# Kernel optimization log

Hardware: AMD Instinct MI355X
Metric: run time of the kernel (lower is better)

Reference implementation:

```python
import jax, jax.numpy as jnp
import numpy as np

N_SRC0, N_DST0 = 100000, 20000   # block0: 100k src -> 20k dst
N_DST1 = 4096                    # block1: 20k src -> 4096 dst (seed nodes)


def setup_inputs() -> dict:
    key = jax.random.key(0)
    ks = jax.random.split(key, 8)
    E0, E1 = 640000, 131072
    return {
        "features": jax.random.normal(ks[0], (N_SRC0, 256), jnp.float32),
        "W1": jax.random.normal(ks[1], (256, 256), jnp.float32) * (1.0 / np.sqrt(256)),
        "b1": jnp.zeros((256,), jnp.float32),
        "W2": jax.random.normal(ks[2], (256, 128), jnp.float32) * (1.0 / np.sqrt(256)),
        "b2": jnp.zeros((128,), jnp.float32),
        "src0": jax.random.randint(ks[3], (E0,), 0, N_SRC0, jnp.int32),
        "dst0": jax.random.randint(ks[4], (E0,), 0, N_DST0, jnp.int32),
        "src1": jax.random.randint(ks[5], (E1,), 0, N_DST0, jnp.int32),
        "dst1": jax.random.randint(ks[6], (E1,), 0, N_DST1, jnp.int32),
    }


def _graph_conv(src, dst, n_dst, feat, W, b):
    # DGL GraphConv, norm='both': D_out^{-1/2} gather-sum D_in^{-1/2}, then WX+b.
    n_src = feat.shape[0]
    ones = jnp.ones(src.shape[0], feat.dtype)
    out_deg = jax.ops.segment_sum(ones, src, num_segments=n_src)
    norm_src = jnp.clip(out_deg, 1.0, None) ** -0.5          # [n_src]
    h = feat * norm_src[:, None]
    agg = jax.ops.segment_sum(h[src], dst, num_segments=n_dst)  # sparse SpMM
    in_deg = jax.ops.segment_sum(ones, dst, num_segments=n_dst)
    norm_dst = jnp.clip(in_deg, 1.0, None) ** -0.5           # [n_dst]
    return (agg * norm_dst[:, None]) @ W + b


def reference(features, W1, b1, W2, b2, src0, dst0, src1, dst1):
    x = jax.nn.relu(_graph_conv(src0, dst0, N_DST0, features, W1, b1))
    x = _graph_conv(src1, dst1, N_DST1, x, W2, b2)
    return x
```

## Files before the change

kernel.cpp:

```cpp
#include <hip/hip_runtime.h>
#include <hip/hip_bf16.h>

#define K_DIM 256
#define RSTRIDE 128
#define EPB 8192

#define G0_DB 625
#define G0_SB 256
#define G0_SW 392
#define G1_DB 128
#define G1_SB 64
#define G1_SW 313

#define NB_FIN (G0_DB + G1_DB + G0_SB + G1_SB)

typedef short bf16x8 __attribute__((ext_vector_type(8)));
typedef float f32x4 __attribute__((ext_vector_type(4)));

static __device__ __forceinline__ unsigned short f2bf(float x) {
    __hip_bfloat16 b = __float2bfloat16(x);
    return *reinterpret_cast<unsigned short*>(&b);
}
static __device__ __forceinline__ float bflo(unsigned int p) {
    return __uint_as_float(p << 16);
}
static __device__ __forceinline__ float bfhi(unsigned int p) {
    return __uint_as_float(p & 0xffff0000u);
}

static __device__ __forceinline__ void block_exscan(
        const int* __restrict__ hist, int* __restrict__ offs, int* __restrict__ tmp, int M) {
    const int tid = threadIdx.x;
    const int S = (M + 255) >> 8;
    const int base = tid * S;
    int sum = 0;
    for (int k = 0; k < S; ++k) {
        int idx = base + k;
        if (idx < M) sum += hist[idx];
    }
    tmp[tid] = sum;
    __syncthreads();
    for (int d = 1; d < 256; d <<= 1) {
        int v = tmp[tid];
        int u = (tid >= d) ? tmp[tid - d] : 0;
        __syncthreads();
        tmp[tid] = v + u;
        __syncthreads();
    }
    int run = (tid == 0) ? 0 : tmp[tid - 1];
    for (int k = 0; k < S; ++k) {
        int idx = base + k;
        if (idx < M) { offs[idx] = run; run += hist[idx]; }
    }
    __syncthreads();
}

struct SplitSh {
    int hist[640];
    int offs[640];
    int tmp[256];
    unsigned sorted[EPB];
};

template <int NDB, int NSB, int SW>
static __device__ __forceinline__ void split_sort(
        const int* __restrict__ src, const int* __restrict__ dst, int E, int chunk,
        int* __restrict__ cntD, int* __restrict__ offD,
        int* __restrict__ cntS, int* __restrict__ offS,
        unsigned* __restrict__ sortD, unsigned* __restrict__ sortS, SplitSh& sh) {
    const int tid = threadIdx.x;
    const int e0 = chunk * EPB;
    const int n = min(EPB, E - e0);
    for (int i = tid; i < NDB; i += 256) sh.hist[i] = 0;
    __syncthreads();
    for (int j = tid; j < n; j += 256) atomicAdd(&sh.hist[dst[e0 + j] >> 5], 1);
    __syncthreads();
    block_exscan(sh.hist, sh.offs, sh.tmp, NDB);
    for (int i = tid; i < NDB; i += 256) {
        cntD[chunk * NDB + i] = sh.hist[i];
        offD[chunk * NDB + i] = sh.offs[i];
    }
    __syncthreads();
    for (int j = tid; j < n; j += 256) {
        int d = dst[e0 + j];
        int s = src[e0 + j];
        int pos = atomicAdd(&sh.offs[d >> 5], 1);
        sh.sorted[pos] = ((unsigned)s << 5) | (unsigned)(d & 31);
    }
    __syncthreads();
    {
        unsigned* __restrict__ gout = sortD + (size_t)chunk * EPB;
        for (int j = tid; j < n; j += 256) gout[j] = sh.sorted[j];
    }
    __syncthreads();
    for (int i = tid; i < NSB; i += 256) sh.hist[i] = 0;
    __syncthreads();
    for (int j = tid; j < n; j += 256)
        atomicAdd(&sh.hist[(int)((unsigned)src[e0 + j] / SW)], 1);
    __syncthreads();
    block_exscan(sh.hist, sh.offs, sh.tmp, NSB);
    for (int i = tid; i < NSB; i += 256) {
        cntS[chunk * NSB + i] = sh.hist[i];
        offS[chunk * NSB + i] = sh.offs[i];
    }
    __syncthreads();
    for (int j = tid; j < n; j += 256) {
        unsigned s = (unsigned)src[e0 + j];
        int pos = atomicAdd(&sh.offs[s / SW], 1);
        sh.sorted[pos] = s;
    }
    __syncthreads();
    {
        unsigned* __restrict__ gout = sortS + (size_t)chunk * EPB;
        for (int j = tid; j < n; j += 256) gout[j] = sh.sorted[j];
    }
}

__global__ __launch_bounds__(256) void splitA_kernel(
        const int* __restrict__ src0, const int* __restrict__ dst0, int E0,
        const int* __restrict__ src1, const int* __restrict__ dst1, int E1,
        int* __restrict__ cntD0, int* __restrict__ offD0,
        int* __restrict__ cntS0, int* __restrict__ offS0,
        unsigned* __restrict__ sortD0, unsigned* __restrict__ sortS0,
        int* __restrict__ cntD1, int* __restrict__ offD1,
        int* __restrict__ cntS1, int* __restrict__ offS1,
        unsigned* __restrict__ sortD1, unsigned* __restrict__ sortS1,
        int nA0, int nA1,
        const float* __restrict__ feat, unsigned short* __restrict__ h, int total_f,
        int castBlocks,
        const float* __restrict__ W1, uint4* __restrict__ pw1,
        const float* __restrict__ W2, uint4* __restrict__ pw2) {
    __shared__ SplitSh sh;
    const int b = blockIdx.x;
    if (b < nA0) {
        split_sort<G0_DB, G0_SB, G0_SW>(src0, dst0, E0, b,
                                        cntD0, offD0, cntS0, offS0, sortD0, sortS0, sh);
    } else if (b < nA0 + nA1) {
        split_sort<G1_DB, G1_SB, G1_SW>(src1, dst1, E1, b - nA0,
                                        cntD1, offD1, cntS1, offS1, sortD1, sortS1, sh);
    } else if (b < nA0 + nA1 + castBlocks) {
        int idx = ((b - nA0 - nA1) * blockDim.x + threadIdx.x) * 8;
        if (idx >= total_f) return;
        const float4 v0 = *reinterpret_cast<const float4*>(feat + idx);
        const float4 v1 = *reinterpret_cast<const float4*>(feat + idx + 4);
        union { ushort4 u4[2]; uint4 u; } o;
        o.u4[0].x = f2bf(v0.x); o.u4[0].y = f2bf(v0.y);
        o.u4[0].z = f2bf(v0.z); o.u4[0].w = f2bf(v0.w);
        o.u4[1].x = f2bf(v1.x); o.u4[1].y = f2bf(v1.y);
        o.u4[1].z = f2bf(v1.z); o.u4[1].w = f2bf(v1.w);
        *reinterpret_cast<uint4*>(h + idx) = o.u;
    } else if (b < nA0 + nA1 + castBlocks + 32) {
        int idx = (b - nA0 - nA1 - castBlocks) * blockDim.x + threadIdx.x;
        int lane = idx & 63;
        int kt = (idx >> 6) & 7;
        int nt = idx >> 9;
        int n = nt * 16 + (lane & 15);
        int k = kt * 32 + (lane >> 4) * 8;
        union { unsigned short us[8]; uint4 u; } o;
#pragma unroll
        for (int j = 0; j < 8; ++j) o.us[j] = f2bf(W1[(size_t)(k + j) * 256 + n]);
        pw1[idx] = o.u;
    } else {
        int idx = (b - nA0 - nA1 - castBlocks - 32) * blockDim.x + threadIdx.x;
        int lane = idx & 63;
        int kt = (idx >> 6) & 7;
        int nt = idx >> 9;
        int n = nt * 16 + (lane & 15);
        int k = kt * 32 + (lane >> 4) * 8;
        union { unsigned short us[8]; uint4 u; } o;
#pragma unroll
        for (int j = 0; j < 8; ++j) o.us[j] = f2bf(W2[(size_t)(k + j) * 128 + n]);
        pw2[idx] = o.u;
    }
}

template <int NDB, int GT>
static __device__ __forceinline__ void fin_dst(
        const unsigned* __restrict__ sortD, const int* __restrict__ cntD,
        const int* __restrict__ offD, int nblk, int b,
        int* __restrict__ esrc, int* __restrict__ cnt, int* tile, int* rowc) {
    const int tid = threadIdx.x;
    if (tid < 32) rowc[tid] = 0;
    __syncthreads();
    for (int rr = tid / GT; rr < nblk; rr += 256 / GT) {
        const int c = cntD[rr * NDB + b];
        const int o = offD[rr * NDB + b];
        const unsigned* __restrict__ seg = sortD + (size_t)rr * EPB + o;
        for (int j = tid % GT; j < c; j += GT) {
            unsigned v = seg[j];
            int dloc = v & 31;
            int s = (int)(v >> 5);
            int slot = atomicAdd(&rowc[dloc], 1);
            if (slot < RSTRIDE) tile[(dloc << 7) + slot] = s;
        }
    }
    __syncthreads();
    int* __restrict__ gout = esrc + ((size_t)b << 12);
    for (int i = tid; i < 32 * RSTRIDE; i += 256) gout[i] = tile[i];
    if (tid < 32) cnt[b * 32 + tid] = rowc[tid];
}

template <int NSB, int SW, int GT>
static __device__ __forceinline__ void fin_src(
        const unsigned* __restrict__ sortS, const int* __restrict__ cntS,
        const int* __restrict__ offS, int nblk, int b, int NN,
        int* __restrict__ od, int* hist) {
    const int tid = threadIdx.x;
    for (int i = tid; i < SW; i += 256) hist[i] = 0;
    __syncthreads();
    const int base = b * SW;
    for (int rr = tid / GT; rr < nblk; rr += 256 / GT) {
        const int c = cntS[rr * NSB + b];
        const int o = offS[rr * NSB + b];
        const unsigned* __restrict__ seg = sortS + (size_t)rr * EPB + o;
        for (int j = tid % GT; j < c; j += GT)
            atomicAdd(&hist[(int)seg[j] - base], 1);
    }
    __syncthreads();
    for (int i = tid; i < SW; i += 256) {
        int node = base + i;
        if (node < NN) od[node] = hist[i];
    }
}

__global__ __launch_bounds__(256) void finalize_kernel(
        int nA0, int nA1,
        const unsigned* __restrict__ sortD0, const int* __restrict__ cntD0,
        const int* __restrict__ offD0, int* __restrict__ cnt0, int* __restrict__ esrc0,
        const unsigned* __restrict__ sortD1, const int* __restrict__ cntD1,
        const int* __restrict__ offD1, int* __restrict__ cnt1, int* __restrict__ esrc1,
        const unsigned* __restrict__ sortS0, const int* __restrict__ cntS0,
        const int* __restrict__ offS0, int* __restrict__ od0,
        const unsigned* __restrict__ sortS1, const int* __restrict__ cntS1,
        const int* __restrict__ offS1, int* __restrict__ od1) {
    __shared__ union {
        struct { int tile[32 * RSTRIDE]; int rowc[32]; } d;
        int hist[G0_SW];
    } sh;
    int b = blockIdx.x;
    if (b < G0_DB) {
        fin_dst<G0_DB, 2>(sortD0, cntD0, offD0, nA0, b, esrc0, cnt0, sh.d.tile, sh.d.rowc);
    } else if (b < G0_DB + G1_DB) {
        fin_dst<G1_DB, 16>(sortD1, cntD1, offD1, nA1, b - G0_DB, esrc1, cnt1,
                           sh.d.tile, sh.d.rowc);
    } else if (b < G0_DB + G1_DB + G0_SB) {
        fin_src<G0_SB, G0_SW, 2>(sortS0, cntS0, offS0, nA0, b - G0_DB - G1_DB,
                                 100000, od0, sh.hist);
    } else {
        fin_src<G1_SB, G1_SW, 16>(sortS1, cntS1, offS1, nA1, b - G0_DB - G1_DB - G0_SB,
                                  20000, od1, sh.hist);
    }
}

template <bool NORM>
static __device__ __forceinline__ void gather4_to_lds(
        const unsigned short* __restrict__ hfeat, const int* __restrict__ esrc,
        const int* __restrict__ cnt, const int* __restrict__ od,
        int m0, int w, int lane, unsigned short (*Alds)[264]) {
#pragma unroll
    for (int k = 0; k < 4; ++k) {
        const int rloc = w * 4 + k;
        const int row = m0 + rloc;
        const int c = cnt[row];
        const int cend = min(c, RSTRIDE);
        const int* __restrict__ ep = esrc + ((size_t)row << 7);
        float a0 = 0.f, a1 = 0.f, a2 = 0.f, a3 = 0.f;
        int i = 0;
        for (; i + 7 < cend; i += 8) {
            int s[8];
            uint2 p[8];
            float nn[8];
#pragma unroll
            for (int u = 0; u < 8; ++u) s[u] = ep[i + u];
#pragma unroll
            for (int u = 0; u < 8; ++u)
                p[u] = *reinterpret_cast<const uint2*>(hfeat + (((size_t)s[u]) << 8) + lane * 4);
#pragma unroll
            for (int u = 0; u < 8; ++u)
                nn[u] = NORM ? rsqrtf((float)max(od[s[u]], 1)) : 1.0f;
#pragma unroll
            for (int u = 0; u < 8; ++u) {
                if (NORM) {
                    a0 = fmaf(bflo(p[u].x), nn[u], a0); a1 = fmaf(bfhi(p[u].x), nn[u], a1);
                    a2 = fmaf(bflo(p[u].y), nn[u], a2); a3 = fmaf(bfhi(p[u].y), nn[u], a3);
                } else {
                    a0 += bflo(p[u].x); a1 += bfhi(p[u].x);
                    a2 += bflo(p[u].y); a3 += bfhi(p[u].y);
                }
            }
        }
        for (; i < cend; ++i) {
            int s0 = ep[i];
            float n0 = NORM ? rsqrtf((float)max(od[s0], 1)) : 1.0f;
            const uint2 p0 = *reinterpret_cast<const uint2*>(hfeat + (((size_t)s0) << 8) + lane * 4);
            if (NORM) {
                a0 = fmaf(bflo(p0.x), n0, a0); a1 = fmaf(bfhi(p0.x), n0, a1);
                a2 = fmaf(bflo(p0.y), n0, a2); a3 = fmaf(bfhi(p0.y), n0, a3);
            } else {
                a0 += bflo(p0.x); a1 += bfhi(p0.x);
                a2 += bflo(p0.y); a3 += bfhi(p0.y);
            }
        }
        float nd = rsqrtf((float)max(c, 1));
        ushort4 o;
        o.x = f2bf(a0 * nd);
        o.y = f2bf(a1 * nd);
        o.z = f2bf(a2 * nd);
        o.w = f2bf(a3 * nd);
        *reinterpret_cast<ushort4*>(&Alds[rloc][lane * 4]) = o;
    }
}

__global__ __launch_bounds__(256) void fused0_kernel(
        const unsigned short* __restrict__ hfeat, const int* __restrict__ esrc,
        const int* __restrict__ cnt, const int* __restrict__ od0,
        const uint4* __restrict__ pW, const float* __restrict__ bias,
        const int* __restrict__ od1, unsigned short* __restrict__ out) {
    __shared__ unsigned short Alds[16][264];
    const int m0 = blockIdx.x * 16;
    const int w = threadIdx.x >> 6;
    const int lane = threadIdx.x & 63;
    gather4_to_lds<true>(hfeat, esrc, cnt, od0, m0, w, lane, Alds);
    __syncthreads();

    bf16x8 a[8];
    const unsigned short* ap = &Alds[lane & 15][(lane >> 4) * 8];
#pragma unroll
    for (int kt = 0; kt < 8; ++kt)
        a[kt] = *reinterpret_cast<const bf16x8*>(ap + kt * 32);

    const int rbase = m0 + (lane >> 4) * 4;
    float nsv[4];
#pragma unroll
    for (int r = 0; r < 4; ++r) nsv[r] = rsqrtf((float)max(od1[rbase + r], 1));

#pragma unroll
    for (int nt = 0; nt < 4; ++nt) {
        const int n0 = w * 64 + nt * 16;
        f32x4 acc = {0.f, 0.f, 0.f, 0.f};
#pragma unroll
        for (int kt = 0; kt < 8; ++kt) {
            bf16x8 b = *reinterpret_cast<const bf16x8*>(&pW[((size_t)(n0 >> 4) * 8 + kt) * 64 + lane]);
            acc = __builtin_amdgcn_mfma_f32_16x16x32_bf16(a[kt], b, acc, 0, 0, 0);
        }
        const int col = n0 + (lane & 15);
        const float bv = bias[col];
#pragma unroll
        for (int r = 0; r < 4; ++r) {
            float v = fmaxf(acc[r] + bv, 0.0f) * nsv[r];
            out[(size_t)(rbase + r) * K_DIM + col] = f2bf(v);
        }
    }
}

__global__ __launch_bounds__(256) void fused1_kernel(
        const unsigned short* __restrict__ xb, const int* __restrict__ esrc,
        const int* __restrict__ cnt,
        const uint4* __restrict__ pW, const float* __restrict__ bias,
        float* __restrict__ out) {
    __shared__ unsigned short Alds[16][264];
    const int m0 = blockIdx.x * 16;
    const int w = threadIdx.x >> 6;
    const int lane = threadIdx.x & 63;
    gather4_to_lds<false>(xb, esrc, cnt, nullptr, m0, w, lane, Alds);
    __syncthreads();

    bf16x8 a[8];
    const unsigned short* ap = &Alds[lane & 15][(lane >> 4) * 8];
#pragma unroll
    for (int kt = 0; kt < 8; ++kt)
        a[kt] = *reinterpret_cast<const bf16x8*>(ap + kt * 32);

    const int rbase = m0 + (lane >> 4) * 4;
#pragma unroll
    for (int nt = 0; nt < 2; ++nt) {
        const int n0 = w * 32 + nt * 16;
        f32x4 acc = {0.f, 0.f, 0.f, 0.f};
#pragma unroll
        for (int kt = 0; kt < 8; ++kt) {
            bf16x8 b = *reinterpret_cast<const bf16x8*>(&pW[((size_t)(n0 >> 4) * 8 + kt) * 64 + lane]);
            acc = __builtin_amdgcn_mfma_f32_16x16x32_bf16(a[kt], b, acc, 0, 0, 0);
        }
        const int col = n0 + (lane & 15);
        const float bv = bias[col];
#pragma unroll
        for (int r = 0; r < 4; ++r)
            out[(size_t)(rbase + r) * 128 + col] = acc[r] + bv;
    }
}

__global__ __launch_bounds__(256) void gatherf_kernel(
        const float* __restrict__ feat, const int* __restrict__ esrc,
        const int* __restrict__ cnt, const int* __restrict__ od,
        float* __restrict__ outbuf, int n_dst) {
    int row = blockIdx.x * (blockDim.x >> 6) + (threadIdx.x >> 6);
    int lane = threadIdx.x & 63;
    if (row >= n_dst) return;
    const int c = cnt[row];
    const int cend = min(c, RSTRIDE);
    const int* __restrict__ ep = esrc + ((size_t)row << 7);
    float4 acc = {0.f, 0.f, 0.f, 0.f};
    for (int i = 0; i < cend; ++i) {
        int s0 = ep[i];
        float n0 = rsqrtf((float)max(od[s0], 1));
        const float4 v0 = *reinterpret_cast<const float4*>(feat + (((size_t)s0) << 8) + lane * 4);
        acc.x = fmaf(v0.x, n0, acc.x); acc.y = fmaf(v0.y, n0, acc.y);
        acc.z = fmaf(v0.z, n0, acc.z); acc.w = fmaf(v0.w, n0, acc.w);
    }
    float nd = rsqrtf((float)max(c, 1));
    float4 o = {acc.x * nd, acc.y * nd, acc.z * nd, acc.w * nd};
    *reinterpret_cast<float4*>(outbuf + (((size_t)row) << 8) + lane * 4) = o;
}

__global__ void edges_kernel(const int* __restrict__ src0, const int* __restrict__ dst0,
                             int* __restrict__ od0, int* __restrict__ cnt0,
                             int* __restrict__ esrc0, int E0,
                             const int* __restrict__ src1, const int* __restrict__ dst1,
                             int* __restrict__ od1, int* __restrict__ cnt1,
                             int* __restrict__ esrc1, int E1) {
    int i = blockIdx.x * blockDim.x + threadIdx.x;
    if (i < E0) {
        int s = src0[i];
        int d = dst0[i];
        atomicAdd(&od0[s], 1);
        int slot = atomicAdd(&cnt0[d], 1);
        if (slot < RSTRIDE) esrc0[(d << 7) + slot] = s;
    } else if (i < E0 + E1) {
        int e = i - E0;
        int s = src1[e];
        int d = dst1[e];
        atomicAdd(&od1[s], 1);
        int slot = atomicAdd(&cnt1[d], 1);
        if (slot < RSTRIDE) esrc1[(d << 7) + slot] = s;
    }
}

template <int ROWS, int NCOLS, bool RELU>
__global__ __launch_bounds__(NCOLS) void gemm_kernel(
        const float* __restrict__ A, const float* __restrict__ W,
        const float* __restrict__ bias, float* __restrict__ out, int M) {
    const int row0 = blockIdx.x * ROWS;
    const int c = threadIdx.x;
    const float* __restrict__ Ablk = A + (size_t)row0 * K_DIM;
    const float* __restrict__ Wc = W + c;

    float acc[ROWS];
#pragma unroll
    for (int r = 0; r < ROWS; ++r) acc[r] = 0.0f;

    float w0 = Wc[0];
    float w1 = Wc[NCOLS];
    float w2 = Wc[2 * NCOLS];
    float w3 = Wc[3 * NCOLS];

#pragma unroll 2
    for (int k = 0; k < K_DIM - 4; k += 4) {
        const float* p = Wc + (size_t)(k + 4) * NCOLS;
        float n0 = p[0];
        float n1 = p[NCOLS];
        float n2 = p[2 * NCOLS];
        float n3 = p[3 * NCOLS];
#pragma unroll
        for (int r = 0; r < ROWS; ++r) {
            const float4 a = *reinterpret_cast<const float4*>(Ablk + r * K_DIM + k);
            acc[r] = fmaf(a.x, w0, acc[r]);
            acc[r] = fmaf(a.y, w1, acc[r]);
            acc[r] = fmaf(a.z, w2, acc[r]);
            acc[r] = fmaf(a.w, w3, acc[r]);
        }
        w0 = n0; w1 = n1; w2 = n2; w3 = n3;
    }
    {
        const int k = K_DIM - 4;
#pragma unroll
        for (int r = 0; r < ROWS; ++r) {
            const float4 a = *reinterpret_cast<const float4*>(Ablk + r * K_DIM + k);
            acc[r] = fmaf(a.x, w0, acc[r]);
            acc[r] = fmaf(a.y, w1, acc[r]);
            acc[r] = fmaf(a.z, w2, acc[r]);
            acc[r] = fmaf(a.w, w3, acc[r]);
        }
    }

    const float b = bias[c];
#pragma unroll
    for (int r = 0; r < ROWS; ++r) {
        float v = acc[r] + b;
        if (RELU) v = fmaxf(v, 0.0f);
        out[(size_t)(row0 + r) * NCOLS + c] = v;
    }
}

extern "C" void kernel_launch(void* const* d_in, const int* in_sizes, int n_in,
                              void* d_out, int out_size, void* d_ws, size_t ws_size,
                              hipStream_t stream) {
    const float* features = (const float*)d_in[0];
    const float* W1 = (const float*)d_in[1];
    const float* b1 = (const float*)d_in[2];
    const float* W2 = (const float*)d_in[3];
    const float* b2 = (const float*)d_in[4];
    const int* src0 = (const int*)d_in[5];
    const int* dst0 = (const int*)d_in[6];
    const int* src1 = (const int*)d_in[7];
    const int* dst1 = (const int*)d_in[8];
    const int E0 = in_sizes[5];
    const int E1 = in_sizes[7];
    const int NSRC0 = 100000, NDST0 = 20000, NDST1 = 4096;
    const int nA0 = (E0 + EPB - 1) / EPB;
    const int nA1 = (E1 + EPB - 1) / EPB;

    char* ws = (char*)d_ws;
    size_t off = 0;
    auto carve = [&](size_t bytes) -> void* {
        void* p = ws + off;
        off = (off + bytes + 255) & ~(size_t)255;
        return p;
    };
    int* od0  = (int*)carve((size_t)NSRC0 * 4);
    int* od1  = (int*)carve((size_t)NDST0 * 4);
    int* cnt0 = (int*)carve((size_t)NDST0 * 4);
    int* cnt1 = (int*)carve((size_t)NDST1 * 4);
    const size_t zero_span = off;
    int* esrc0p = (int*)carve((size_t)NDST0 * RSTRIDE * 4);
    int* esrc1p = (int*)carve((size_t)NDST1 * RSTRIDE * 4);
    uint4* pW1  = (uint4*)carve((size_t)8192 * 16);
    uint4* pW2  = (uint4*)carve((size_t)4096 * 16);
    int* cntD0 = (int*)carve((size_t)nA0 * G0_DB * 4);
    int* offD0 = (int*)carve((size_t)nA0 * G0_DB * 4);
    int* cntS0 = (int*)carve((size_t)nA0 * G0_SB * 4);
    int* offS0 = (int*)carve((size_t)nA0 * G0_SB * 4);
    int* cntD1 = (int*)carve((size_t)nA1 * G1_DB * 4);
    int* offD1 = (int*)carve((size_t)nA1 * G1_DB * 4);
    int* cntS1 = (int*)carve((size_t)nA1 * G1_SB * 4);
    int* offS1 = (int*)carve((size_t)nA1 * G1_SB * 4);
    unsigned* sortD0 = (unsigned*)carve((size_t)nA0 * EPB * 4);
    unsigned* sortS0 = (unsigned*)carve((size_t)nA0 * EPB * 4);
    unsigned* sortD1 = (unsigned*)carve((size_t)nA1 * EPB * 4);
    unsigned* sortS1 = (unsigned*)carve((size_t)nA1 * EPB * 4);
    unsigned short* xbufb = (unsigned short*)carve((size_t)NDST0 * K_DIM * 2);
    unsigned short* hfeat = (unsigned short*)carve((size_t)NSRC0 * K_DIM * 2);
    const size_t need_bf16 = off;
    (void)n_in; (void)out_size;

    if (ws_size >= need_bf16) {
        const int total_f = NSRC0 * K_DIM;
        const int castBlocks = (total_f / 8 + 255) / 256;
        splitA_kernel<<<nA0 + nA1 + castBlocks + 48, 256, 0, stream>>>(
            src0, dst0, E0, src1, dst1, E1,
            cntD0, offD0, cntS0, offS0, sortD0, sortS0,
            cntD1, offD1, cntS1, offS1, sortD1, sortS1,
            nA0, nA1, features, hfeat, total_f, castBlocks,
            W1, pW1, W2, pW2);
        finalize_kernel<<<NB_FIN, 256, 0, stream>>>(
            nA0, nA1,
            sortD0, cntD0, offD0, cnt0, esrc0p,
            sortD1, cntD1, offD1, cnt1, esrc1p,
            sortS0, cntS0, offS0, od0,
            sortS1, cntS1, offS1, od1);
        fused0_kernel<<<NDST0 / 16, 256, 0, stream>>>(
            hfeat, esrc0p, cnt0, od0, pW1, b1, od1, xbufb);
        fused1_kernel<<<NDST1 / 16, 256, 0, stream>>>(
            xbufb, esrc1p, cnt1, pW2, b2, (float*)d_out);
    } else {
        hipMemsetAsync(ws, 0, zero_span, stream);
        float* agg0 = (float*)carve((size_t)NDST0 * K_DIM * 4);
        float* xbuf = (float*)carve((size_t)NDST0 * K_DIM * 4);
        float* agg1 = (float*)carve((size_t)NDST1 * K_DIM * 4);
        edges_kernel<<<(E0 + E1 + 255) / 256, 256, 0, stream>>>(
            src0, dst0, od0, cnt0, esrc0p, E0,
            src1, dst1, od1, cnt1, esrc1p, E1);
        gatherf_kernel<<<(NDST0 + 3) / 4, 256, 0, stream>>>(features, esrc0p, cnt0, od0,
                                                            agg0, NDST0);
        gemm_kernel<16, 256, true><<<NDST0 / 16, 256, 0, stream>>>(agg0, W1, b1, xbuf, NDST0);
        gatherf_kernel<<<(NDST1 + 3) / 4, 256, 0, stream>>>(xbuf, esrc1p, cnt1, od1,
                                                            agg1, NDST1);
        gemm_kernel<4, 128, false><<<NDST1 / 4, 128, 0, stream>>>(agg1, W2, b2,
                                                                  (float*)d_out, NDST1);
    }
}
```

Baseline: 296.3 us.

## Precompute source-degree norms in finalize and use 512-thread fused blocks

The finalize kernel now writes rsqrt(max(deg,1)) as floats instead of raw out-degree ints, so the gather loop does one load per edge instead of a load plus rsqrt. The fused gather+MFMA kernels move from 256 to 512 threads per 16-row block. Each wave now gathers 2 rows instead of 4 and computes half as many output column tiles. This gives more waves in flight to hide latency on the random feature gathers, at the cost of higher register pressure under launch_bounds(512,8).

```diff
diff --git a/kernel.cpp b/kernel.cpp
--- a/kernel.cpp
+++ b/kernel.cpp
@@ -204,7 +204,7 @@
 static __device__ __forceinline__ void fin_src(
         const unsigned* __restrict__ sortS, const int* __restrict__ cntS,
         const int* __restrict__ offS, int nblk, int b, int NN,
-        int* __restrict__ od, int* hist) {
+        float* __restrict__ nv, int* hist) {
     const int tid = threadIdx.x;
     for (int i = tid; i < SW; i += 256) hist[i] = 0;
     __syncthreads();
@@ -219,7 +219,7 @@
     __syncthreads();
     for (int i = tid; i < SW; i += 256) {
         int node = base + i;
-        if (node < NN) od[node] = hist[i];
+        if (node < NN) nv[node] = rsqrtf((float)max(hist[i], 1));
     }
 }
 
@@ -230,9 +230,9 @@
         const unsigned* __restrict__ sortD1, const int* __restrict__ cntD1,
         const int* __restrict__ offD1, int* __restrict__ cnt1, int* __restrict__ esrc1,
         const unsigned* __restrict__ sortS0, const int* __restrict__ cntS0,
-        const int* __restrict__ offS0, int* __restrict__ od0,
+        const int* __restrict__ offS0, float* __restrict__ nv0,
         const unsigned* __restrict__ sortS1, const int* __restrict__ cntS1,
-        const int* __restrict__ offS1, int* __restrict__ od1) {
+        const int* __restrict__ offS1, float* __restrict__ nv1) {
     __shared__ union {
         struct { int tile[32 * RSTRIDE]; int rowc[32]; } d;
         int hist[G0_SW];
@@ -245,21 +245,21 @@
                            sh.d.tile, sh.d.rowc);
     } else if (b < G0_DB + G1_DB + G0_SB) {
         fin_src<G0_SB, G0_SW, 2>(sortS0, cntS0, offS0, nA0, b - G0_DB - G1_DB,
-                                 100000, od0, sh.hist);
+                                 100000, nv0, sh.hist);
     } else {
         fin_src<G1_SB, G1_SW, 16>(sortS1, cntS1, offS1, nA1, b - G0_DB - G1_DB - G0_SB,
-                                  20000, od1, sh.hist);
+                                  20000, nv1, sh.hist);
     }
 }
 
 template <bool NORM>
-static __device__ __forceinline__ void gather4_to_lds(
+static __device__ __forceinline__ void gather2_to_lds(
         const unsigned short* __restrict__ hfeat, const int* __restrict__ esrc,
-        const int* __restrict__ cnt, const int* __restrict__ od,
+        const int* __restrict__ cnt, const float* __restrict__ nv,
         int m0, int w, int lane, unsigned short (*Alds)[264]) {
 #pragma unroll
-    for (int k = 0; k < 4; ++k) {
-        const int rloc = w * 4 + k;
+    for (int k = 0; k < 2; ++k) {
+        const int rloc = w * 2 + k;
         const int row = m0 + rloc;
         const int c = cnt[row];
         const int cend = min(c, RSTRIDE);
@@ -277,7 +277,7 @@
                 p[u] = *reinterpret_cast<const uint2*>(hfeat + (((size_t)s[u]) << 8) + lane * 4);
 #pragma unroll
             for (int u = 0; u < 8; ++u)
-                nn[u] = NORM ? rsqrtf((float)max(od[s[u]], 1)) : 1.0f;
+                nn[u] = NORM ? nv[s[u]] : 1.0f;
 #pragma unroll
             for (int u = 0; u < 8; ++u) {
                 if (NORM) {
@@ -291,7 +291,7 @@
         }
         for (; i < cend; ++i) {
             int s0 = ep[i];
-            float n0 = NORM ? rsqrtf((float)max(od[s0], 1)) : 1.0f;
+            float n0 = NORM ? nv[s0] : 1.0f;
             const uint2 p0 = *reinterpret_cast<const uint2*>(hfeat + (((size_t)s0) << 8) + lane * 4);
             if (NORM) {
                 a0 = fmaf(bflo(p0.x), n0, a0); a1 = fmaf(bfhi(p0.x), n0, a1);
@@ -311,16 +311,16 @@
     }
 }
 
-__global__ __launch_bounds__(256) void fused0_kernel(
+__global__ __launch_bounds__(512, 8) void fused0_kernel(
         const unsigned short* __restrict__ hfeat, const int* __restrict__ esrc,
-        const int* __restrict__ cnt, const int* __restrict__ od0,
+        const int* __restrict__ cnt, const float* __restrict__ nv0,
         const uint4* __restrict__ pW, const float* __restrict__ bias,
-        const int* __restrict__ od1, unsigned short* __restrict__ out) {
+        const float* __restrict__ nv1, unsigned short* __restrict__ out) {
     __shared__ unsigned short Alds[16][264];
     const int m0 = blockIdx.x * 16;
     const int w = threadIdx.x >> 6;
     const int lane = threadIdx.x & 63;
-    gather4_to_lds<true>(hfeat, esrc, cnt, od0, m0, w, lane, Alds);
+    gather2_to_lds<true>(hfeat, esrc, cnt, nv0, m0, w, lane, Alds);
     __syncthreads();
 
     bf16x8 a[8];
@@ -332,11 +332,11 @@
     const int rbase = m0 + (lane >> 4) * 4;
     float nsv[4];
 #pragma unroll
-    for (int r = 0; r < 4; ++r) nsv[r] = rsqrtf((float)max(od1[rbase + r], 1));
-
-#pragma unroll
-    for (int nt = 0; nt < 4; ++nt) {
-        const int n0 = w * 64 + nt * 16;
+    for (int r = 0; r < 4; ++r) nsv[r] = nv1[rbase + r];
+
+#pragma unroll
+    for (int nt = 0; nt < 2; ++nt) {
+        const int n0 = w * 32 + nt * 16;
         f32x4 acc = {0.f, 0.f, 0.f, 0.f};
 #pragma unroll
         for (int kt = 0; kt < 8; ++kt) {
@@ -353,7 +353,7 @@
     }
 }
 
-__global__ __launch_bounds__(256) void fused1_kernel(
+__global__ __launch_bounds__(512, 8) void fused1_kernel(
         const unsigned short* __restrict__ xb, const int* __restrict__ esrc,
         const int* __restrict__ cnt,
         const uint4* __restrict__ pW, const float* __restrict__ bias,
@@ -362,7 +362,7 @@
     const int m0 = blockIdx.x * 16;
     const int w = threadIdx.x >> 6;
     const int lane = threadIdx.x & 63;
-    gather4_to_lds<false>(xb, esrc, cnt, nullptr, m0, w, lane, Alds);
+    gather2_to_lds<false>(xb, esrc, cnt, nullptr, m0, w, lane, Alds);
     __syncthreads();
 
     bf16x8 a[8];
@@ -372,9 +372,8 @@
         a[kt] = *reinterpret_cast<const bf16x8*>(ap + kt * 32);
 
     const int rbase = m0 + (lane >> 4) * 4;
-#pragma unroll
-    for (int nt = 0; nt < 2; ++nt) {
-        const int n0 = w * 32 + nt * 16;
+    {
+        const int n0 = w * 16;
         f32x4 acc = {0.f, 0.f, 0.f, 0.f};
 #pragma unroll
         for (int kt = 0; kt < 8; ++kt) {
@@ -543,6 +542,8 @@
     (void)n_in; (void)out_size;
 
     if (ws_size >= need_bf16) {
+        float* nv0 = (float*)od0;
+        float* nv1 = (float*)od1;
         const int total_f = NSRC0 * K_DIM;
         const int castBlocks = (total_f / 8 + 255) / 256;
         splitA_kernel<<<nA0 + nA1 + castBlocks + 48, 256, 0, stream>>>(
@@ -555,11 +556,11 @@
             nA0, nA1,
             sortD0, cntD0, offD0, cnt0, esrc0p,
             sortD1, cntD1, offD1, cnt1, esrc1p,
-            sortS0, cntS0, offS0, od0,
-            sortS1, cntS1, offS1, od1);
-        fused0_kernel<<<NDST0 / 16, 256, 0, stream>>>(
-            hfeat, esrc0p, cnt0, od0, pW1, b1, od1, xbufb);
-        fused1_kernel<<<NDST1 / 16, 256, 0, stream>>>(
+            sortS0, cntS0, offS0, nv0,
+            sortS1, cntS1, offS1, nv1);
+        fused0_kernel<<<NDST0 / 16, 512, 0, stream>>>(
+            hfeat, esrc0p, cnt0, nv0, pW1, b1, nv1, xbufb);
+        fused1_kernel<<<NDST1 / 16, 512, 0, stream>>>(
             xbufb, esrc1p, cnt1, pW2, b2, (float*)d_out);
     } else {
         hipMemsetAsync(ws, 0, zero_span, stream);
```

Measured after the change: 279.7 us. 5.6% less time.
